# Optimization experiments

Hardware: AMD Instinct MI355X
Metric: run time of the kernel (lower is better)

Reference implementation:

```python
import jax, jax.numpy as jnp
import numpy as np

B = 262144
IN = 256
HID = 128
OUT = 15
C = 15  # num_cameras


def setup_inputs() -> dict:
    key = jax.random.key(0)
    k_x, k_c, k_w1, k_b1, k_w2, k_b2 = jax.random.split(key, 6)
    x = jax.random.normal(k_x, (B, IN), dtype=jnp.float32)
    cam = jax.random.randint(k_c, (B,), 0, C)
    # per-camera 2-layer MLP params (Linear->ReLU->Dropout(eval)->Linear)
    W1 = jax.random.normal(k_w1, (C, IN, HID), dtype=jnp.float32) / np.sqrt(IN)
    b1 = jax.random.normal(k_b1, (C, HID), dtype=jnp.float32) * 0.01
    W2 = jax.random.normal(k_w2, (C, HID, OUT), dtype=jnp.float32) / np.sqrt(HID)
    b2 = jax.random.normal(k_b2, (C, OUT), dtype=jnp.float32) * 0.01
    return {"input": x, "cam": cam, "W1": W1, "b1": b1, "W2": W2, "b2": b2}


def reference(input, cam, W1, b1, W2, b2):
    # Per-sample camera-id dispatch to one of C small MLPs, vectorized:
    # run each camera's MLP on the full batch (C is small/fixed) and select
    # each sample's output by its camera id. Dropout is identity (eval mode).
    out = jnp.zeros((input.shape[0], OUT), dtype=input.dtype)
    for c in range(C):
        h = jax.nn.relu(input @ W1[c] + b1[c])      # [B, HID]
        logits = h @ W2[c] + b2[c]                  # [B, OUT]
        out = jnp.where((cam == c)[:, None], logits, out)
    return out
```

## Files before the change

### kernel.cpp

```cpp
#include <hip/hip_runtime.h>
#include <hip/hip_bf16.h>

#define BB    262144
#define INF   256
#define HIDF  128
#define OUTF  15
#define NCAM  15
#define TM    128
#define MAXTILES (BB/TM + NCAM)

typedef __attribute__((ext_vector_type(8))) short          bf16x8;
typedef __attribute__((ext_vector_type(4))) float          floatx4;
typedef __attribute__((ext_vector_type(4))) int            intx4;
typedef __attribute__((ext_vector_type(4))) unsigned int   uintx4;
typedef __attribute__((ext_vector_type(8))) unsigned short ushortx8;

__device__ __forceinline__ unsigned short f2bf1(float a){
  unsigned int u = __builtin_bit_cast(unsigned int, a);
  u += 0x7fffu + ((u >> 16) & 1u);
  return (unsigned short)(u >> 16);
}
__device__ __forceinline__ unsigned int f2bf2(float a, float b){
  return (unsigned int)f2bf1(a) | ((unsigned int)f2bf1(b) << 16);
}

__global__ void k_prephist(const float* __restrict__ W1, const float* __restrict__ W2,
                           const int* __restrict__ cam,
                           unsigned short* __restrict__ W1p, unsigned short* __restrict__ W2p,
                           int* __restrict__ counts){
  int bid = blockIdx.x, tid = threadIdx.x;
  if (bid < 240){
    int t = bid * 256 + tid;
    int l  = t & 63;
    int kf = (t >> 6) & 7;
    int nf = (t >> 9) & 7;
    int c  = t >> 12;
    int col = nf*16 + (l & 15);
    int k0  = kf*32 + (l >> 4)*8;
    ushortx8 v;
    #pragma unroll
    for (int j = 0; j < 8; ++j)
      v[j] = f2bf1(W1[((size_t)c*INF + k0 + j)*HIDF + col]);
    *reinterpret_cast<ushortx8*>(W1p + (size_t)t*8) = v;
  } else if (bid < 255){
    int c  = bid - 240;
    int l  = tid & 63;
    int kf = tid >> 6;
    int col = l & 15;
    int k0  = kf*32 + (l >> 4)*8;
    ushortx8 v;
    #pragma unroll
    for (int j = 0; j < 8; ++j){
      float f = (col < OUTF) ? W2[((size_t)c*HIDF + k0 + j)*OUTF + col] : 0.0f;
      v[j] = f2bf1(f);
    }
    *reinterpret_cast<ushortx8*>(W2p + ((size_t)(c*4 + kf)*64 + l)*8) = v;
  } else if (bid >= 256){
    __shared__ int lc[NCAM];
    if (tid < NCAM) lc[tid] = 0;
    __syncthreads();
    intx4 v = *reinterpret_cast<const intx4*>(cam + (size_t)((bid-256)*256 + tid)*4);
    atomicAdd(&lc[v[0]], 1); atomicAdd(&lc[v[1]], 1);
    atomicAdd(&lc[v[2]], 1); atomicAdd(&lc[v[3]], 1);
    __syncthreads();
    if (tid < NCAM && lc[tid]) atomicAdd(&counts[tid], lc[tid]);
  }
}

__global__ void k_scatter(const int* __restrict__ cam, const int* __restrict__ counts,
                          int* __restrict__ scatterOfs, int* __restrict__ idx){
  __shared__ int lc[NCAM];
  __shared__ int loff[NCAM];
  __shared__ int base[NCAM];
  int t = threadIdx.x;
  if (t < NCAM) lc[t] = 0;
  __syncthreads();
  int start = blockIdx.x * 4096;
  int camr[16], lpos[16];
  #pragma unroll
  for (int j = 0; j < 16; ++j){
    int i = start + j*256 + t;
    camr[j] = cam[i];
    lpos[j] = atomicAdd(&lc[camr[j]], 1);
  }
  __syncthreads();
  if (t == 0){
    int s = 0;
    #pragma unroll
    for (int c = 0; c < NCAM; ++c){ loff[c] = s; s += counts[c]; }
  }
  __syncthreads();
  if (t < NCAM) base[t] = loff[t] + atomicAdd(&scatterOfs[t], lc[t]);
  __syncthreads();
  #pragma unroll
  for (int j = 0; j < 16; ++j)
    idx[base[camr[j]] + lpos[j]] = start + j*256 + t;
}

__global__ __launch_bounds__(256, 2) void k_mlp(
    const float* __restrict__ x, const int* __restrict__ idx,
    const int* __restrict__ counts,
    const unsigned short* __restrict__ W1p, const unsigned short* __restrict__ W2p,
    const float* __restrict__ b1, const float* __restrict__ b2,
    float* __restrict__ out)
{
  __shared__ __align__(16) char smem[65536];

  int bid = blockIdx.x;
  int c = -1, segStart = 0, rowStart = 0, rows = 0;
  {
    int cum = 0, rcum = 0;
    #pragma unroll 1
    for (int cc = 0; cc < NCAM; ++cc){
      int n  = counts[cc];
      int nt = (n + TM - 1) / TM;
      if (c < 0 && bid < cum + nt){
        c = cc;
        rowStart = (bid - cum) * TM;
        segStart = rcum;
        rows = n - rowStart; if (rows > TM) rows = TM;
      }
      cum += nt; rcum += n;
    }
  }
  if (c < 0) return;

  int t = threadIdx.x;
  int wave = t >> 6, lane = t & 63;
  int wr  = wave * 32;
  int l15 = lane & 15, lk = lane >> 4;
  const int* idxBase = idx + segStart + rowStart;

  const char* srcp[8];
  {
    int rowsel = lane >> 4;
    int w = (lane & 15) * 16;
    #pragma unroll
    for (int i = 0; i < 8; ++i){
      int row = wr + i*4 + rowsel;
      int rc = (row < rows) ? row : (rows - 1);
      int g = idxBase[rc];
      int offr = w ^ (((i*4 + rowsel) & 7) << 4);
      srcp[i] = reinterpret_cast<const char*>(x) + (size_t)g*1024 + offr;
    }
  }

  #define STAGE(q) { \
    char* dbase = smem + ((q)&1)*32768 + wave*8192; \
    _Pragma("unroll") \
    for (int i = 0; i < 8; ++i){ \
      __builtin_amdgcn_global_load_lds( \
        (const __attribute__((address_space(1))) unsigned int*)(srcp[i] + (q)*256), \
        (__attribute__((address_space(3))) unsigned int*)(dbase + i*1024), \
        16, 0, 0); \
    } \
  }

  const unsigned short* bbase = W1p + (size_t)c*32768 + lane*8;

  floatx4 acc[2][8];
  #pragma unroll
  for (int i = 0; i < 2; ++i)
    #pragma unroll
    for (int j = 0; j < 8; ++j) acc[i][j] = (floatx4)0.0f;

  bf16x8 bfr[2][8];

  STAGE(0);
  #pragma unroll
  for (int nf = 0; nf < 8; ++nf)
    bfr[0][nf] = *reinterpret_cast<const bf16x8*>(bbase + nf*4096);
  __syncthreads();

  int swz = (l15 & 7) << 4;

  #pragma unroll
  for (int q = 0; q < 4; ++q){
    if (q < 3) STAGE(q+1);
    #pragma unroll
    for (int kfl = 0; kfl < 2; ++kfl){
      const int kf = q*2 + kfl;
      if (kf < 7){
        #pragma unroll
        for (int nf = 0; nf < 8; ++nf)
          bfr[(kf+1)&1][nf] = *reinterpret_cast<const bf16x8*>(bbase + nf*4096 + (kf+1)*512);
      }
      bf16x8 af[2];
      #pragma unroll
      for (int mf = 0; mf < 2; ++mf){
        int row = wr + mf*16 + l15;
        const char* rbase = smem + (q&1)*32768 + row*256;
        int w1 = kfl*128 + lk*32;
        floatx4 f0 = *reinterpret_cast<const floatx4*>(rbase + (w1 ^ swz));
        floatx4 f1 = *reinterpret_cast<const floatx4*>(rbase + ((w1+16) ^ swz));
        uintx4 u;
        u[0] = f2bf2(f0[0], f0[1]); u[1] = f2bf2(f0[2], f0[3]);
        u[2] = f2bf2(f1[0], f1[1]); u[3] = f2bf2(f1[2], f1[3]);
        af[mf] = __builtin_bit_cast(bf16x8, u);
      }
      #pragma unroll
      for (int nf = 0; nf < 8; ++nf)
        acc[0][nf] = __builtin_amdgcn_mfma_f32_16x16x32_bf16(af[0], bfr[kf&1][nf], acc[0][nf], 0, 0, 0);
      #pragma unroll
      for (int nf = 0; nf < 8; ++nf)
        acc[1][nf] = __builtin_amdgcn_mfma_f32_16x16x32_bf16(af[1], bfr[kf&1][nf], acc[1][nf], 0, 0, 0);
    }
    __syncthreads();
  }

  #pragma unroll
  for (int nf = 0; nf < 8; ++nf){
    int col = nf*16 + l15;
    float bias = b1[c*HIDF + col];
    #pragma unroll
    for (int mf = 0; mf < 2; ++mf){
      #pragma unroll
      for (int j = 0; j < 4; ++j){
        int row = wr + mf*16 + lk*4 + j;
        float h = fmaxf(acc[mf][nf][j] + bias, 0.0f);
        int off = row*256 + ((col*2) ^ ((row & 7) << 4));
        *reinterpret_cast<unsigned short*>(smem + off) = f2bf1(h);
      }
    }
  }
  __syncthreads();

  floatx4 acc2[2];
  acc2[0] = (floatx4)0.0f; acc2[1] = (floatx4)0.0f;
  const unsigned short* wb = W2p + (size_t)c*2048 + lane*8;
  #pragma unroll
  for (int kf = 0; kf < 4; ++kf){
    bf16x8 wv = *reinterpret_cast<const bf16x8*>(wb + kf*512);
    #pragma unroll
    for (int mf = 0; mf < 2; ++mf){
      int row = wr + mf*16 + l15;
      int off = row*256 + ((kf*64 + lk*16) ^ ((row & 7) << 4));
      bf16x8 av = *reinterpret_cast<const bf16x8*>(smem + off);
      acc2[mf] = __builtin_amdgcn_mfma_f32_16x16x32_bf16(av, wv, acc2[mf], 0, 0, 0);
    }
  }

  int col = l15;
  if (col < OUTF){
    float bias2 = b2[c*OUTF + col];
    #pragma unroll
    for (int mf = 0; mf < 2; ++mf){
      #pragma unroll
      for (int j = 0; j < 4; ++j){
        int r = wr + mf*16 + lk*4 + j;
        if (r < rows)
          out[(size_t)idxBase[r]*OUTF + col] = acc2[mf][j] + bias2;
      }
    }
  }
  #undef STAGE
}

extern "C" void kernel_launch(void* const* d_in, const int* in_sizes, int n_in,
                              void* d_out, int out_size, void* d_ws, size_t ws_size,
                              hipStream_t stream) {
  const float* x  = (const float*)d_in[0];
  const int*   cam= (const int*)d_in[1];
  const float* W1 = (const float*)d_in[2];
  const float* b1 = (const float*)d_in[3];
  const float* W2 = (const float*)d_in[4];
  const float* b2 = (const float*)d_in[5];
  float* out = (float*)d_out;

  char* ws = (char*)d_ws;
  int* counts     = (int*)(ws);
  int* scatterOfs = (int*)(ws + 64);
  int* idx        = (int*)(ws + 256);
  unsigned short* W1p = (unsigned short*)(ws + 256 + (size_t)BB*4);
  unsigned short* W2p = W1p + (size_t)NCAM*8*8*64*8;

  (void)hipMemsetAsync(counts, 0, 128, stream);
  hipLaunchKernelGGL(k_prephist, dim3(512),     dim3(256), 0, stream, W1, W2, cam, W1p, W2p, counts);
  hipLaunchKernelGGL(k_scatter,  dim3(BB/4096), dim3(256), 0, stream, cam, counts, scatterOfs, idx);
  hipLaunchKernelGGL(k_mlp,      dim3(MAXTILES),dim3(256), 0, stream,
                     x, idx, counts, W1p, W2p, b1, b2, out);
}
```

Before: 95.52 us.

## Use per-wave 4-stage async LDS pipeline with vmcnt waits, drop block barriers

Replaces the block-wide double-buffered 256-byte K staging with a per-wave 4-deep ring of 128-byte K slices, issued three stages ahead and gated by explicit s_waitcnt vmcnt counts instead of __syncthreads. Each wave touches only its own LDS region, so the hidden-layer writeback and the second GEMM also run without block barriers. The counts prefix scan is vectorized and fully unrolled. The aim is more loads in flight and less barrier stalling. The hand-tuned vmcnt values depend on the exact order of issued loads, so they are fragile to compiler scheduling.

```diff
diff --git a/kernel.cpp b/kernel.cpp
--- a/kernel.cpp
+++ b/kernel.cpp
@@ -107,13 +107,19 @@
   __shared__ __align__(16) char smem[65536];
 
   int bid = blockIdx.x;
+  intx4 q0 = *reinterpret_cast<const intx4*>(counts);
+  intx4 q1 = *reinterpret_cast<const intx4*>(counts + 4);
+  intx4 q2 = *reinterpret_cast<const intx4*>(counts + 8);
+  intx4 q3 = *reinterpret_cast<const intx4*>(counts + 12);
+  int cnt[16] = {q0[0],q0[1],q0[2],q0[3], q1[0],q1[1],q1[2],q1[3],
+                 q2[0],q2[1],q2[2],q2[3], q3[0],q3[1],q3[2],q3[3]};
   int c = -1, segStart = 0, rowStart = 0, rows = 0;
   {
     int cum = 0, rcum = 0;
-    #pragma unroll 1
+    #pragma unroll
     for (int cc = 0; cc < NCAM; ++cc){
-      int n  = counts[cc];
-      int nt = (n + TM - 1) / TM;
+      int n  = cnt[cc];
+      int nt = (n + TM - 1) >> 7;
       if (c < 0 && bid < cum + nt){
         c = cc;
         rowStart = (bid - cum) * TM;
@@ -127,36 +133,32 @@
 
   int t = threadIdx.x;
   int wave = t >> 6, lane = t & 63;
-  int wr  = wave * 32;
-  int l15 = lane & 15, lk = lane >> 4;
+  int wr  = wave * 32, l15 = lane & 15, lk = lane >> 4;
   const int* idxBase = idx + segStart + rowStart;
 
-  const char* srcp[8];
+  const char* srcp[4];
   {
-    int rowsel = lane >> 4;
-    int w = (lane & 15) * 16;
-    #pragma unroll
-    for (int i = 0; i < 8; ++i){
-      int row = wr + i*4 + rowsel;
+    int sr = lane >> 3, su = lane & 7;
+    int woff = (su ^ sr) * 16;
+    #pragma unroll
+    for (int i = 0; i < 4; ++i){
+      int row = wr + i*8 + sr;
       int rc = (row < rows) ? row : (rows - 1);
-      int g = idxBase[rc];
-      int offr = w ^ (((i*4 + rowsel) & 7) << 4);
-      srcp[i] = reinterpret_cast<const char*>(x) + (size_t)g*1024 + offr;
-    }
-  }
-
-  #define STAGE(q) { \
-    char* dbase = smem + ((q)&1)*32768 + wave*8192; \
+      srcp[i] = reinterpret_cast<const char*>(x) + (size_t)idxBase[rc]*1024 + woff;
+    }
+  }
+
+  const unsigned short* bbase = W1p + (size_t)c*32768 + lane*8;
+
+#define STAGE(qq) { \
+    char* db = smem + ((qq)&3)*16384 + wave*4096; \
     _Pragma("unroll") \
-    for (int i = 0; i < 8; ++i){ \
+    for (int i = 0; i < 4; ++i){ \
       __builtin_amdgcn_global_load_lds( \
-        (const __attribute__((address_space(1))) unsigned int*)(srcp[i] + (q)*256), \
-        (__attribute__((address_space(3))) unsigned int*)(dbase + i*1024), \
+        (const __attribute__((address_space(1))) unsigned int*)(srcp[i] + (qq)*128), \
+        (__attribute__((address_space(3))) unsigned int*)(db + i*1024), \
         16, 0, 0); \
-    } \
-  }
-
-  const unsigned short* bbase = W1p + (size_t)c*32768 + lane*8;
+    } }
 
   floatx4 acc[2][8];
   #pragma unroll
@@ -165,47 +167,50 @@
     for (int j = 0; j < 8; ++j) acc[i][j] = (floatx4)0.0f;
 
   bf16x8 bfr[2][8];
-
-  STAGE(0);
   #pragma unroll
   for (int nf = 0; nf < 8; ++nf)
     bfr[0][nf] = *reinterpret_cast<const bf16x8*>(bbase + nf*4096);
-  __syncthreads();
-
-  int swz = (l15 & 7) << 4;
-
-  #pragma unroll
-  for (int q = 0; q < 4; ++q){
-    if (q < 3) STAGE(q+1);
-    #pragma unroll
-    for (int kfl = 0; kfl < 2; ++kfl){
-      const int kf = q*2 + kfl;
-      if (kf < 7){
-        #pragma unroll
-        for (int nf = 0; nf < 8; ++nf)
-          bfr[(kf+1)&1][nf] = *reinterpret_cast<const bf16x8*>(bbase + nf*4096 + (kf+1)*512);
-      }
-      bf16x8 af[2];
-      #pragma unroll
-      for (int mf = 0; mf < 2; ++mf){
-        int row = wr + mf*16 + l15;
-        const char* rbase = smem + (q&1)*32768 + row*256;
-        int w1 = kfl*128 + lk*32;
-        floatx4 f0 = *reinterpret_cast<const floatx4*>(rbase + (w1 ^ swz));
-        floatx4 f1 = *reinterpret_cast<const floatx4*>(rbase + ((w1+16) ^ swz));
-        uintx4 u;
-        u[0] = f2bf2(f0[0], f0[1]); u[1] = f2bf2(f0[2], f0[3]);
-        u[2] = f2bf2(f1[0], f1[1]); u[3] = f2bf2(f1[2], f1[3]);
-        af[mf] = __builtin_bit_cast(bf16x8, u);
-      }
+  __builtin_amdgcn_sched_barrier(0);
+  STAGE(0); STAGE(1); STAGE(2);
+  __builtin_amdgcn_sched_barrier(0);
+
+  int swz8 = l15 & 7;
+
+  #pragma unroll
+  for (int kf = 0; kf < 8; ++kf){
+    if (kf < 7){
       #pragma unroll
       for (int nf = 0; nf < 8; ++nf)
-        acc[0][nf] = __builtin_amdgcn_mfma_f32_16x16x32_bf16(af[0], bfr[kf&1][nf], acc[0][nf], 0, 0, 0);
-      #pragma unroll
-      for (int nf = 0; nf < 8; ++nf)
-        acc[1][nf] = __builtin_amdgcn_mfma_f32_16x16x32_bf16(af[1], bfr[kf&1][nf], acc[1][nf], 0, 0, 0);
-    }
-    __syncthreads();
+        bfr[(kf+1)&1][nf] = *reinterpret_cast<const bf16x8*>(bbase + nf*4096 + (kf+1)*512);
+    }
+    __builtin_amdgcn_sched_barrier(0);
+    if (kf < 5) STAGE(kf+3);
+    __builtin_amdgcn_sched_barrier(0);
+    if (kf == 0)      asm volatile("s_waitcnt vmcnt(20)" ::: "memory");
+    else if (kf <= 4) asm volatile("s_waitcnt vmcnt(16)" ::: "memory");
+    else if (kf == 5) asm volatile("s_waitcnt vmcnt(12)" ::: "memory");
+    else if (kf == 6) asm volatile("s_waitcnt vmcnt(8)"  ::: "memory");
+    else              asm volatile("s_waitcnt vmcnt(0)"  ::: "memory");
+    __builtin_amdgcn_sched_barrier(0);
+
+    bf16x8 af[2];
+    #pragma unroll
+    for (int mf = 0; mf < 2; ++mf){
+      int rl = mf*16 + l15;
+      const char* rb = smem + (kf&3)*16384 + wave*4096 + rl*128;
+      floatx4 f0 = *reinterpret_cast<const floatx4*>(rb + (((2*lk)   ^ swz8) * 16));
+      floatx4 f1 = *reinterpret_cast<const floatx4*>(rb + (((2*lk+1) ^ swz8) * 16));
+      uintx4 u;
+      u[0] = f2bf2(f0[0], f0[1]); u[1] = f2bf2(f0[2], f0[3]);
+      u[2] = f2bf2(f1[0], f1[1]); u[3] = f2bf2(f1[2], f1[3]);
+      af[mf] = __builtin_bit_cast(bf16x8, u);
+    }
+    #pragma unroll
+    for (int nf = 0; nf < 8; ++nf)
+      acc[0][nf] = __builtin_amdgcn_mfma_f32_16x16x32_bf16(af[0], bfr[kf&1][nf], acc[0][nf], 0, 0, 0);
+    #pragma unroll
+    for (int nf = 0; nf < 8; ++nf)
+      acc[1][nf] = __builtin_amdgcn_mfma_f32_16x16x32_bf16(af[1], bfr[kf&1][nf], acc[1][nf], 0, 0, 0);
   }
 
   #pragma unroll
@@ -216,14 +221,13 @@
     for (int mf = 0; mf < 2; ++mf){
       #pragma unroll
       for (int j = 0; j < 4; ++j){
-        int row = wr + mf*16 + lk*4 + j;
+        int rl = mf*16 + lk*4 + j;
         float h = fmaxf(acc[mf][nf][j] + bias, 0.0f);
-        int off = row*256 + ((col*2) ^ ((row & 7) << 4));
+        int off = (rl>>4)*16384 + wave*4096 + (rl&15)*256 + ((col*2) ^ ((rl&7)<<4));
         *reinterpret_cast<unsigned short*>(smem + off) = f2bf1(h);
       }
     }
   }
-  __syncthreads();
 
   floatx4 acc2[2];
   acc2[0] = (floatx4)0.0f; acc2[1] = (floatx4)0.0f;
@@ -233,8 +237,8 @@
     bf16x8 wv = *reinterpret_cast<const bf16x8*>(wb + kf*512);
     #pragma unroll
     for (int mf = 0; mf < 2; ++mf){
-      int row = wr + mf*16 + l15;
-      int off = row*256 + ((kf*64 + lk*16) ^ ((row & 7) << 4));
+      int rl = mf*16 + l15;
+      int off = (rl>>4)*16384 + wave*4096 + (rl&15)*256 + ((kf*64 + lk*16) ^ ((rl&7)<<4));
       bf16x8 av = *reinterpret_cast<const bf16x8*>(smem + off);
       acc2[mf] = __builtin_amdgcn_mfma_f32_16x16x32_bf16(av, wv, acc2[mf], 0, 0, 0);
     }
@@ -253,7 +257,7 @@
       }
     }
   }
-  #undef STAGE
+#undef STAGE
 }
 
 extern "C" void kernel_launch(void* const* d_in, const int* in_sizes, int n_in,
```

New measurement: 93.49 us, median of 2. 1.02x faster.
